# Kernel tuning notes

Hardware: AMD Instinct MI355X
Metric: run time of the kernel (lower is better)

## Reference

```python
import jax, jax.numpy as jnp
import numpy as np

N_HEADS = 8
D_EMBED = 64
B, S = 2, 2048
ROPE_BASE = 10000.0


def apply_rope(x):
    # x: [b, h, s, d]; interleaved-pair rotary embedding over the s axis
    d = x.shape[-1]
    s = x.shape[-2]
    inv_freq = 1.0 / (ROPE_BASE ** (jnp.arange(0, d, 2, dtype=jnp.float32) / d))  # [d/2]
    angles = jnp.arange(s, dtype=jnp.float32)[:, None] * inv_freq[None, :]  # [s, d/2]
    cos = jnp.cos(angles)[None, None, :, :]
    sin = jnp.sin(angles)[None, None, :, :]
    x1 = x[..., 0::2]
    x2 = x[..., 1::2]
    out = jnp.stack([x1 * cos - x2 * sin, x1 * sin + x2 * cos], axis=-1)
    return out.reshape(x.shape)


def setup_inputs() -> dict:
    key = jax.random.key(0)
    ks = jax.random.split(key, 7)
    scale = 1.0 / np.sqrt(D_EMBED)
    return {
        "q": jax.random.normal(ks[0], (B, S, D_EMBED), dtype=jnp.float32),
        "k": jax.random.normal(ks[1], (B, S, D_EMBED), dtype=jnp.float32),
        "v": jax.random.normal(ks[2], (B, S, D_EMBED), dtype=jnp.float32),
        "W_q": jax.random.normal(ks[3], (N_HEADS, D_EMBED, D_EMBED), dtype=jnp.float32) * scale,
        "W_k": jax.random.normal(ks[4], (N_HEADS, D_EMBED, D_EMBED), dtype=jnp.float32) * scale,
        "W_v": jax.random.normal(ks[5], (N_HEADS, D_EMBED, D_EMBED), dtype=jnp.float32) * scale,
        "W_o": jax.random.normal(ks[6], (N_HEADS * D_EMBED, D_EMBED), dtype=jnp.float32) * scale,
    }


def reference(q, k, v, W_q, W_k, W_v, W_o):
    Bn, Sn, E = q.shape
    H = W_q.shape[0]
    qh = jnp.einsum('bsz,hzd->bhsd', q, W_q)
    kh = jnp.einsum('bsz,hzd->bhsd', k, W_k)
    vh = jnp.einsum('bsz,hzd->bhsd', v, W_v)
    qh = apply_rope(qh)
    kh = apply_rope(kh)
    attn_scaling = 1.0 / E  # note: 1/d, not 1/sqrt(d), per original
    scores = jnp.einsum('bhqd,bhkd->bhqk', qh, kh)
    causal = jnp.triu(jnp.ones((Sn, Sn), dtype=bool), k=1)
    scores = jnp.where(causal[None, None], -jnp.inf, scores) * attn_scaling
    probs = jax.nn.softmax(scores, axis=-1)
    # post-softmax diagonal zeroing (breaks normalization; this is the ICL twist)
    diag_mask = 1.0 - jnp.eye(Sn, dtype=probs.dtype)
    probs = probs * diag_mask[None, None]
    # NOTE: einsum 'bhzs,bhzd->bhsd' in the original contracts over the QUERY axis
    # (probs transposed): out[k-pos] = sum_q P[q, k-pos] * v[q]
    out = jnp.einsum('bhqk,bhqd->bhkd', probs, vh)
    out = out.transpose(0, 2, 1, 3).reshape(Bn, Sn, H * E)
    return jnp.einsum('bsz,zd->bsd', out, W_o)
```

## Files before the change

### kernel.cpp

```cpp
#include <hip/hip_runtime.h>
#include <hip/hip_bf16.h>
#include <math.h>

#define NH 8
#define D 64
#define BB 2
#define SS 2048
#define NBH (BB*NH)
#define LOG2E 1.4426950408889634f
#define KPAR 8
#define QPAR 4

typedef short bf16x8 __attribute__((ext_vector_type(8)));
typedef float f32x4 __attribute__((ext_vector_type(4)));

#define MFMA16(a,b,c) __builtin_amdgcn_mfma_f32_16x16x32_bf16((a),(b),(c),0,0,0)

__device__ inline short f2bf(float f) {
    unsigned u = __float_as_uint(f);
    unsigned r = (u + 0x7fffu + ((u >> 16) & 1u)) >> 16;
    return (short)r;
}
__device__ inline float bf2f(short s) {
    return __uint_as_float(((unsigned)(unsigned short)s) << 16);
}
__device__ inline unsigned pack2bf(float a, float b) {
    __hip_bfloat162 hv = __float22bfloat162_rn(make_float2(a, b));
    unsigned u;
    __builtin_memcpy(&u, &hv, 4);
    return u;
}

__global__ __launch_bounds__(256) void wtrans_kernel(
    const float* __restrict__ Wq, const float* __restrict__ Wk,
    const float* __restrict__ Wv, const float* __restrict__ Wo,
    short* __restrict__ WqT, short* __restrict__ WkT, short* __restrict__ WvT,
    short* __restrict__ WoT) {
    int blk = blockIdx.x;
    int t = threadIdx.x;
    if (blk < 24) {
        int tensor = blk >> 3, h = blk & 7;
        const float* W = tensor == 0 ? Wq : (tensor == 1 ? Wk : Wv);
        short* WT = tensor == 0 ? WqT : (tensor == 1 ? WkT : WvT);
        __shared__ float wl[64][65];
        {
            int z = t >> 2, c0 = (t & 3) * 16;
            const float* src = W + (size_t)h * 4096 + (size_t)z * 64 + c0;
#pragma unroll
            for (int i = 0; i < 16; ++i) wl[z][c0 + i] = src[i];
        }
        __syncthreads();
        {
            int d = t >> 2, z0 = (t & 3) * 16;
            short* dst = WT + ((size_t)h * 64 + d) * 64 + z0;
#pragma unroll
            for (int i = 0; i < 16; ++i) dst[i] = f2bf(wl[z0 + i][d]);
        }
    } else {
        int idx = (blk - 24) * 256 + t;
        int d = idx >> 6;
        int zc = (idx & 63) * 32;
#pragma unroll
        for (int j = 0; j < 32; ++j) {
            int z = zc + j;
            WoT[(size_t)d * 2048 + z] = f2bf(Wo[(size_t)(z & 511) * 64 + d]);
        }
    }
}

__global__ __launch_bounds__(256) void proj_mfma_kernel(
    const float* __restrict__ xq, const float* __restrict__ xk,
    const float* __restrict__ xv,
    const short* __restrict__ WqT, const short* __restrict__ WkT,
    const short* __restrict__ WvT,
    short* __restrict__ qh, short* __restrict__ kh, short* __restrict__ vhT) {
    int blk = blockIdx.x;
    int tensor = blk / (NBH * 32);
    int rem = blk - tensor * (NBH * 32);
    int st = rem & 31, bh = rem >> 5;
    int h = bh & 7, b = bh >> 3;
    const float* x = tensor == 0 ? xq : (tensor == 1 ? xk : xv);
    const short* WT = tensor == 0 ? WqT : (tensor == 1 ? WkT : WvT);

    int t = threadIdx.x, w = t >> 6, lane = t & 63;
    int l15 = lane & 15, lg = lane >> 4;

    __shared__ short vt[64 * 64];

    int sA = st * 64 + w * 16 + l15;
    const float* xr = x + ((size_t)b * SS + sA) * D + lg * 8;
    bf16x8 a0, a1;
#pragma unroll
    for (int j = 0; j < 8; ++j) a0[j] = f2bf(xr[j]);
#pragma unroll
    for (int j = 0; j < 8; ++j) a1[j] = f2bf(xr[32 + j]);

    bf16x8 bfr[4][2];
#pragma unroll
    for (int ds_ = 0; ds_ < 4; ++ds_) {
        int d = ds_ * 16 + l15;
        const short* wp = WT + ((size_t)h * 64 + d) * 64 + lg * 8;
        bfr[ds_][0] = *(const bf16x8*)(wp);
        bfr[ds_][1] = *(const bf16x8*)(wp + 32);
    }

    f32x4 c[4];
#pragma unroll
    for (int ds_ = 0; ds_ < 4; ++ds_) {
        f32x4 z = {0.f, 0.f, 0.f, 0.f};
        z = MFMA16(a0, bfr[ds_][0], z);
        z = MFMA16(a1, bfr[ds_][1], z);
        c[ds_] = z;
    }

    int sbase = st * 64 + w * 16 + lg * 4;
    if (tensor < 2) {
        short* dst = tensor == 0 ? qh : kh;
        float scale = tensor == 0 ? (LOG2E / 64.0f) : 1.0f;
#pragma unroll
        for (int ds_ = 0; ds_ < 4; ++ds_) {
            int d = ds_ * 16 + l15;
            float invf = exp2f(-(float)(d & ~1) * (13.287712379549449f / 64.0f));
#pragma unroll
            for (int r = 0; r < 4; ++r) {
                float v = c[ds_][r];
                float pr = __shfl_xor(v, 1);
                float ang = (float)(sbase + r) * invf;
                float cs = __cosf(ang), sn = __sinf(ang);
                float o = (d & 1) ? (pr * sn + v * cs) : (v * cs - pr * sn);
                dst[((size_t)bh * SS + sbase + r) * D + d] = f2bf(o * scale);
            }
        }
    } else {
#pragma unroll
        for (int ds_ = 0; ds_ < 4; ++ds_) {
            int d = ds_ * 16 + l15;
#pragma unroll
            for (int r = 0; r < 4; ++r) {
                int sc = w * 16 + lg * 4 + r;
                vt[d * 64 + (sc ^ ((d & 7) << 3))] = f2bf(c[ds_][r]);
            }
        }
        __syncthreads();
#pragma unroll
        for (int pp = 0; pp < 2; ++pp) {
            int idx = pp * 256 + t;
            int d = idx >> 3, a = idx & 7;
            bf16x8 val = *(const bf16x8*)&vt[d * 64 + ((a ^ (d & 7)) << 3)];
            *(bf16x8*)&vhT[((size_t)bh * D + d) * SS + st * 64 + a * 8] = val;
        }
    }
}

__global__ __launch_bounds__(256, 4) void colstats_kernel(
    const short* __restrict__ qh, const short* __restrict__ kh,
    float* __restrict__ lpart) {
    int blk = blockIdx.x;
    int ph2 = blk & 1, qt = (blk >> 1) & 31, bh = blk >> 6;
    int t = threadIdx.x, w = t >> 6, lane = t & 63;
    int l15 = lane & 15, lg = lane >> 4;
    int pp = ph2 * 4 + w;

    bf16x8 qb[4][2];
#pragma unroll
    for (int qs = 0; qs < 4; ++qs) {
        const short* qp = qh + ((size_t)bh * SS + qt * 64 + qs * 16 + l15) * D + lg * 8;
        qb[qs][0] = *(const bf16x8*)qp;
        qb[qs][1] = *(const bf16x8*)(qp + 32);
    }

    const short* kbase = kh + (size_t)bh * SS * D;
    float lsum[4] = {0.f, 0.f, 0.f, 0.f};

    for (int kt = pp; kt <= qt; kt += KPAR) {
        bool diag = (kt == qt);
#pragma unroll
        for (int ks = 0; ks < 4; ++ks) {
            const short* kp = kbase + (size_t)(kt * 64 + ks * 16 + l15) * D + lg * 8;
            bf16x8 ka0 = *(const bf16x8*)kp;
            bf16x8 ka1 = *(const bf16x8*)(kp + 32);
            int kb = kt * 64 + ks * 16 + lg * 4;
#pragma unroll
            for (int qs = 0; qs < 4; ++qs) {
                f32x4 s = {0.f, 0.f, 0.f, 0.f};
                s = MFMA16(ka0, qb[qs][0], s);
                s = MFMA16(ka1, qb[qs][1], s);
                int qc = qt * 64 + qs * 16 + l15;
#pragma unroll
                for (int r = 0; r < 4; ++r) {
                    float e = (!diag || kb + r <= qc) ? exp2f(s[r]) : 0.f;
                    lsum[qs] += e;
                }
            }
        }
    }
#pragma unroll
    for (int qs = 0; qs < 4; ++qs) {
        lsum[qs] += __shfl_xor(lsum[qs], 16);
        lsum[qs] += __shfl_xor(lsum[qs], 32);
    }
    if (lane < 16) {
#pragma unroll
        for (int qs = 0; qs < 4; ++qs)
            lpart[((size_t)pp * NBH + bh) * SS + qt * 64 + qs * 16 + lane] = lsum[qs];
    }
}

__global__ __launch_bounds__(256) void merge_scale_kernel(
    const float* __restrict__ lpart, short* __restrict__ vhT) {
    int blk = blockIdx.x;
    int qc = blk & 15, bh = blk >> 4;
    int t = threadIdx.x;
    const size_t STR = (size_t)NBH * SS;
    __shared__ float il[128];
    if (t < 128) {
        size_t idx = (size_t)bh * SS + qc * 128 + t;
        float l = 0.f;
#pragma unroll
        for (int pp = 0; pp < KPAR; ++pp) l += lpart[pp * STR + idx];
        il[t] = 1.0f / l;
    }
    __syncthreads();
    int d = t >> 2, sub = t & 3;
    size_t base = ((size_t)bh * 64 + d) * SS + qc * 128 + sub * 32;
#pragma unroll
    for (int j = 0; j < 32; j += 8) {
        bf16x8 v = *(bf16x8*)&vhT[base + j];
#pragma unroll
        for (int jj = 0; jj < 8; ++jj)
            v[jj] = f2bf(bf2f(v[jj]) * il[sub * 32 + j + jj]);
        *(bf16x8*)&vhT[base + j] = v;
    }
}

__global__ __launch_bounds__(256, 4) void pv_kernel(
    const short* __restrict__ qh, const short* __restrict__ kh,
    const short* __restrict__ vhT,
    short* __restrict__ attc) {
    int blk = blockIdx.x;
    int ph = blk & 3, p = (blk >> 2) & 15, bh = blk >> 6;
    int h = bh & 7, b = bh >> 3;
    int t = threadIdx.x, w = t >> 6, lane = t & 63;
    int l15 = lane & 15, lg = lane >> 4;
    int kt = (w & 1) ? (31 - p) : p;
    int hf = w >> 1;
    int row0 = kt * 64 + hf * 32;

    __shared__ short pl[4][32 * 64];
    short* plw = pl[w];

    bf16x8 kb[2][2];
#pragma unroll
    for (int kg = 0; kg < 2; ++kg) {
        const short* kp = kh + ((size_t)bh * SS + row0 + kg * 16 + l15) * D + lg * 8;
        kb[kg][0] = *(const bf16x8*)kp;
        kb[kg][1] = *(const bf16x8*)(kp + 32);
    }

    f32x4 acc[2][4];
#pragma unroll
    for (int rg = 0; rg < 2; ++rg)
#pragma unroll
        for (int i = 0; i < 4; ++i) acc[rg][i] = (f32x4){0.f, 0.f, 0.f, 0.f};

    const short* qbase = qh + (size_t)bh * SS * D;
    const short* vbase = vhT + (size_t)bh * D * SS;

    int qt0 = kt + ((ph - kt) & (QPAR - 1));
    for (int qt = qt0; qt < 32; qt += QPAR) {
        bool diag = (qt == kt);
        bf16x8 qa[4][2];
#pragma unroll
        for (int qg = 0; qg < 4; ++qg) {
            const short* qp2 = qbase + (size_t)(qt * 64 + qg * 16 + l15) * D + lg * 8;
            qa[qg][0] = *(const bf16x8*)qp2;
            qa[qg][1] = *(const bf16x8*)(qp2 + 32);
        }
#pragma unroll
        for (int qg = 0; qg < 4; ++qg) {
#pragma unroll
            for (int kg = 0; kg < 2; ++kg) {
                f32x4 s = {0.f, 0.f, 0.f, 0.f};
                s = MFMA16(qa[qg][0], kb[kg][0], s);
                s = MFMA16(qa[qg][1], kb[kg][1], s);
                float p0 = exp2f(s[0]);
                float p1 = exp2f(s[1]);
                float p2 = exp2f(s[2]);
                float p3 = exp2f(s[3]);
                if (diag) {
                    int qoff = qg * 16 + 4 * lg;
                    int kk = hf * 32 + kg * 16 + l15;
                    if (qoff + 0 <= kk) p0 = 0.f;
                    if (qoff + 1 <= kk) p1 = 0.f;
                    if (qoff + 2 <= kk) p2 = 0.f;
                    if (qoff + 3 <= kk) p3 = 0.f;
                }
                unsigned u0 = pack2bf(p0, p1);
                unsigned u1 = pack2bf(p2, p3);
                int row = kg * 16 + l15;
                int col = (qg * 16 + 4 * lg) ^ ((row & 7) << 3);
                uint2 val;
                val.x = u0;
                val.y = u1;
                *(uint2*)&plw[row * 64 + col] = val;
            }
        }
#pragma unroll
        for (int qhh = 0; qhh < 2; ++qhh) {
            int chunk = (qhh << 2) | lg;
            int cc = (chunk ^ (l15 & 7)) << 3;
            bf16x8 pa0 = *(const bf16x8*)&plw[l15 * 64 + cc];
            bf16x8 pa1 = *(const bf16x8*)&plw[(16 + l15) * 64 + cc];
#pragma unroll
            for (int ds_ = 0; ds_ < 4; ++ds_) {
                const short* vp2 = vbase + (size_t)(ds_ * 16 + l15) * SS + qt * 64 + chunk * 8;
                bf16x8 vb = *(const bf16x8*)vp2;
                acc[0][ds_] = MFMA16(pa0, vb, acc[0][ds_]);
                acc[1][ds_] = MFMA16(pa1, vb, acc[1][ds_]);
            }
        }
    }
#pragma unroll
    for (int rg = 0; rg < 2; ++rg)
#pragma unroll
        for (int ds_ = 0; ds_ < 4; ++ds_) {
            int d = ds_ * 16 + l15;
#pragma unroll
            for (int r = 0; r < 4; ++r) {
                int k = row0 + rg * 16 + lg * 4 + r;
                attc[((size_t)b * SS + k) * 2048 + ph * 512 + h * 64 + d] =
                    f2bf(acc[rg][ds_][r]);
            }
        }
}

__global__ __launch_bounds__(256) void outproj_kernel(
    const short* __restrict__ attc, const short* __restrict__ WoT,
    float* __restrict__ out) {
    int blk = blockIdx.x;
    int t = threadIdx.x, w = t >> 6, lane = t & 63;
    int l15 = lane & 15, lg = lane >> 4;
    int srow = blk * 16 + l15;
    const short* arow = attc + (size_t)srow * 2048 + lg * 8;

    f32x4 acc[4];
#pragma unroll
    for (int i = 0; i < 4; ++i) acc[i] = (f32x4){0.f, 0.f, 0.f, 0.f};

#pragma unroll
    for (int i = 0; i < 16; ++i) {
        int kc = w * 16 + i;
        bf16x8 af = *(const bf16x8*)(arow + kc * 32);
#pragma unroll
        for (int ds_ = 0; ds_ < 4; ++ds_) {
            bf16x8 bf_ = *(const bf16x8*)&WoT[(size_t)(ds_ * 16 + l15) * 2048 + kc * 32 + lg * 8];
            acc[ds_] = MFMA16(af, bf_, acc[ds_]);
        }
    }
    __shared__ float red[4][16 * 64];
#pragma unroll
    for (int ds_ = 0; ds_ < 4; ++ds_)
#pragma unroll
        for (int r = 0; r < 4; ++r)
            red[w][(lg * 4 + r) * 64 + ds_ * 16 + l15] = acc[ds_][r];
    __syncthreads();
    {
        int idx4 = t * 4;
        int row = idx4 >> 6, col = idx4 & 63;
        float4 s0 = *(const float4*)&red[0][row * 64 + col];
        float4 s1 = *(const float4*)&red[1][row * 64 + col];
        float4 s2 = *(const float4*)&red[2][row * 64 + col];
        float4 s3 = *(const float4*)&red[3][row * 64 + col];
        float4 sum;
        sum.x = s0.x + s1.x + s2.x + s3.x;
        sum.y = s0.y + s1.y + s2.y + s3.y;
        sum.z = s0.z + s1.z + s2.z + s3.z;
        sum.w = s0.w + s1.w + s2.w + s3.w;
        *(float4*)&out[(size_t)(blk * 16 + row) * 64 + col] = sum;
    }
}

extern "C" void kernel_launch(void* const* d_in, const int* in_sizes, int n_in,
                              void* d_out, int out_size, void* d_ws, size_t ws_size,
                              hipStream_t stream) {
    const float* q  = (const float*)d_in[0];
    const float* k  = (const float*)d_in[1];
    const float* v  = (const float*)d_in[2];
    const float* Wq = (const float*)d_in[3];
    const float* Wk = (const float*)d_in[4];
    const float* Wv = (const float*)d_in[5];
    const float* Wo = (const float*)d_in[6];
    float* out = (float*)d_out;

    const size_t PROJ = (size_t)NBH * SS * D;

    short* qh  = (short*)d_ws;
    short* kh  = qh + PROJ;
    short* vhT = kh + PROJ;
    short* WqT = vhT + PROJ;
    short* WkT = WqT + 32768;
    short* WvT = WkT + 32768;
    short* WoT = WvT + 32768;
    float* lpart = (float*)(WoT + 131072);
    short* attc  = (short*)(lpart + (size_t)KPAR * NBH * SS);

    wtrans_kernel<<<40, 256, 0, stream>>>(Wq, Wk, Wv, Wo, WqT, WkT, WvT, WoT);

    proj_mfma_kernel<<<3 * NBH * 32, 256, 0, stream>>>(q, k, v, WqT, WkT, WvT,
                                                       qh, kh, vhT);

    colstats_kernel<<<NBH * 64, 256, 0, stream>>>(qh, kh, lpart);

    merge_scale_kernel<<<NBH * 16, 256, 0, stream>>>(lpart, vhT);

    pv_kernel<<<NBH * 64, 256, 0, stream>>>(qh, kh, vhT, attc);

    outproj_kernel<<<256, 256, 0, stream>>>(attc, WoT, out);
}
```

Measured before the change: 103.5 us.

## Split colstats and PV work across more blocks with in-block wave reduction

KPAR is doubled so colstats launches twice as many blocks, each covering a finer stride of key tiles and writing more partial sums. pv_kernel now gives each block a single key tile rather than pairing kt with 31-kt. Two waves per row-half take interleaved query-tile classes (stride 8), and their accumulators are summed through LDS before the bf16 store. This raises the block count and shortens per-block serial loops. In exchange it drops the triangular load-balancing pairing, adds an LDS reduction with two barriers, and makes merge_scale read more partials.

```diff
diff --git a/kernel.cpp b/kernel.cpp
--- a/kernel.cpp
+++ b/kernel.cpp
@@ -8,8 +8,8 @@
 #define SS 2048
 #define NBH (BB*NH)
 #define LOG2E 1.4426950408889634f
-#define KPAR 8
-#define QPAR 4
+#define KPAR 16
+#define QCLS 8
 
 typedef short bf16x8 __attribute__((ext_vector_type(8)));
 typedef float f32x4 __attribute__((ext_vector_type(4)));
@@ -156,10 +156,10 @@
     const short* __restrict__ qh, const short* __restrict__ kh,
     float* __restrict__ lpart) {
     int blk = blockIdx.x;
-    int ph2 = blk & 1, qt = (blk >> 1) & 31, bh = blk >> 6;
+    int ph4 = blk & 3, qt = (blk >> 2) & 31, bh = blk >> 7;
     int t = threadIdx.x, w = t >> 6, lane = t & 63;
     int l15 = lane & 15, lg = lane >> 4;
-    int pp = ph2 * 4 + w;
+    int pp = ph4 * 4 + w;
 
     bf16x8 qb[4][2];
 #pragma unroll
@@ -238,12 +238,12 @@
     const short* __restrict__ vhT,
     short* __restrict__ attc) {
     int blk = blockIdx.x;
-    int ph = blk & 3, p = (blk >> 2) & 15, bh = blk >> 6;
+    int ph = blk & 3, kt = (blk >> 2) & 31, bh = blk >> 7;
     int h = bh & 7, b = bh >> 3;
     int t = threadIdx.x, w = t >> 6, lane = t & 63;
     int l15 = lane & 15, lg = lane >> 4;
-    int kt = (w & 1) ? (31 - p) : p;
-    int hf = w >> 1;
+    int sp = w & 1, hf = w >> 1;
+    int qcls = ph * 2 + sp;
     int row0 = kt * 64 + hf * 32;
 
     __shared__ short pl[4][32 * 64];
@@ -266,8 +266,8 @@
     const short* qbase = qh + (size_t)bh * SS * D;
     const short* vbase = vhT + (size_t)bh * D * SS;
 
-    int qt0 = kt + ((ph - kt) & (QPAR - 1));
-    for (int qt = qt0; qt < 32; qt += QPAR) {
+    int qt0 = kt + ((qcls - kt) & (QCLS - 1));
+    for (int qt = qt0; qt < 32; qt += QCLS) {
         bool diag = (qt == kt);
         bf16x8 qa[4][2];
 #pragma unroll
@@ -320,18 +320,36 @@
             }
         }
     }
-#pragma unroll
-    for (int rg = 0; rg < 2; ++rg)
-#pragma unroll
-        for (int ds_ = 0; ds_ < 4; ++ds_) {
-            int d = ds_ * 16 + l15;
-#pragma unroll
-            for (int r = 0; r < 4; ++r) {
-                int k = row0 + rg * 16 + lg * 4 + r;
-                attc[((size_t)b * SS + k) * 2048 + ph * 512 + h * 64 + d] =
-                    f2bf(acc[rg][ds_][r]);
-            }
-        }
+
+    __syncthreads();
+    float* plf = (float*)pl;
+    if (sp == 1) {
+#pragma unroll
+        for (int rg = 0; rg < 2; ++rg)
+#pragma unroll
+            for (int ds_ = 0; ds_ < 4; ++ds_) {
+                int d = ds_ * 16 + l15;
+#pragma unroll
+                for (int r = 0; r < 4; ++r)
+                    plf[hf * 2048 + (rg * 16 + lg * 4 + r) * 64 + d] = acc[rg][ds_][r];
+            }
+    }
+    __syncthreads();
+    if (sp == 0) {
+#pragma unroll
+        for (int rg = 0; rg < 2; ++rg)
+#pragma unroll
+            for (int ds_ = 0; ds_ < 4; ++ds_) {
+                int d = ds_ * 16 + l15;
+#pragma unroll
+                for (int r = 0; r < 4; ++r) {
+                    int lrow = rg * 16 + lg * 4 + r;
+                    float sum = acc[rg][ds_][r] + plf[hf * 2048 + lrow * 64 + d];
+                    int k = row0 + lrow;
+                    attc[((size_t)b * SS + k) * 2048 + ph * 512 + h * 64 + d] = f2bf(sum);
+                }
+            }
+    }
 }
 
 __global__ __launch_bounds__(256) void outproj_kernel(
@@ -409,11 +427,11 @@
     proj_mfma_kernel<<<3 * NBH * 32, 256, 0, stream>>>(q, k, v, WqT, WkT, WvT,
                                                        qh, kh, vhT);
 
-    colstats_kernel<<<NBH * 64, 256, 0, stream>>>(qh, kh, lpart);
+    colstats_kernel<<<NBH * 128, 256, 0, stream>>>(qh, kh, lpart);
 
     merge_scale_kernel<<<NBH * 16, 256, 0, stream>>>(lpart, vhT);
 
-    pv_kernel<<<NBH * 64, 256, 0, stream>>>(qh, kh, vhT, attc);
+    pv_kernel<<<NBH * 128, 256, 0, stream>>>(qh, kh, vhT, attc);
 
     outproj_kernel<<<256, 256, 0, stream>>>(attc, WoT, out);
 }
```

Result: slower. 117.6 us (+13.6%).

## Double-buffer K/Q loads and split pv query range across waves with LDS reduction

Applied to the files above, without the earlier changes.

The row-sum kernel now double-buffers K tile loads so the next tile's global reads are issued before the current tile's MFMAs and exp2. The pv kernel is restructured so each block processes both the kt=p and kt=31-p tiles in sequence. Pairs of waves split the query tiles into 8 classes and their partial accumulators are reduced through shared memory before the bf16 store, with half of each Q tile prefetched ahead. The aim is to hide memory latency and balance causal work, at the cost of extra syncthreads, LDS traffic and register pressure.

```diff
diff --git a/kernel.cpp b/kernel.cpp
--- a/kernel.cpp
+++ b/kernel.cpp
@@ -9,7 +9,7 @@
 #define NBH (BB*NH)
 #define LOG2E 1.4426950408889634f
 #define KPAR 8
-#define QPAR 4
+#define QCLS 8
 
 typedef short bf16x8 __attribute__((ext_vector_type(8)));
 typedef float f32x4 __attribute__((ext_vector_type(4)));
@@ -172,19 +172,24 @@
     const short* kbase = kh + (size_t)bh * SS * D;
     float lsum[4] = {0.f, 0.f, 0.f, 0.f};
 
-    for (int kt = pp; kt <= qt; kt += KPAR) {
-        bool diag = (kt == qt);
+    auto load_k = [&](bf16x8 (&ka)[4][2], int kt) {
 #pragma unroll
         for (int ks = 0; ks < 4; ++ks) {
             const short* kp = kbase + (size_t)(kt * 64 + ks * 16 + l15) * D + lg * 8;
-            bf16x8 ka0 = *(const bf16x8*)kp;
-            bf16x8 ka1 = *(const bf16x8*)(kp + 32);
+            ka[ks][0] = *(const bf16x8*)kp;
+            ka[ks][1] = *(const bf16x8*)(kp + 32);
+        }
+    };
+    auto compute = [&](bf16x8 (&ka)[4][2], int kt) {
+        bool diag = (kt == qt);
+#pragma unroll
+        for (int ks = 0; ks < 4; ++ks) {
             int kb = kt * 64 + ks * 16 + lg * 4;
 #pragma unroll
             for (int qs = 0; qs < 4; ++qs) {
                 f32x4 s = {0.f, 0.f, 0.f, 0.f};
-                s = MFMA16(ka0, qb[qs][0], s);
-                s = MFMA16(ka1, qb[qs][1], s);
+                s = MFMA16(ka[ks][0], qb[qs][0], s);
+                s = MFMA16(ka[ks][1], qb[qs][1], s);
                 int qc = qt * 64 + qs * 16 + l15;
 #pragma unroll
                 for (int r = 0; r < 4; ++r) {
@@ -192,6 +197,24 @@
                     lsum[qs] += e;
                 }
             }
+        }
+    };
+
+    bf16x8 kaA[4][2], kaB[4][2];
+    int kt = pp;
+    if (kt <= qt) {
+        load_k(kaA, kt);
+        while (true) {
+            int ktn = kt + KPAR;
+            if (ktn <= qt) load_k(kaB, ktn);
+            compute(kaA, kt);
+            kt = ktn;
+            if (kt > qt) break;
+            ktn = kt + KPAR;
+            if (ktn <= qt) load_k(kaA, ktn);
+            compute(kaB, kt);
+            kt = ktn;
+            if (kt > qt) break;
         }
     }
 #pragma unroll
@@ -242,96 +265,152 @@
     int h = bh & 7, b = bh >> 3;
     int t = threadIdx.x, w = t >> 6, lane = t & 63;
     int l15 = lane & 15, lg = lane >> 4;
-    int kt = (w & 1) ? (31 - p) : p;
-    int hf = w >> 1;
-    int row0 = kt * 64 + hf * 32;
+    int qsub = w & 1, hf = w >> 1;
+    int qcls = ph * 2 + qsub;
 
     __shared__ short pl[4][32 * 64];
     short* plw = pl[w];
-
-    bf16x8 kb[2][2];
-#pragma unroll
-    for (int kg = 0; kg < 2; ++kg) {
-        const short* kp = kh + ((size_t)bh * SS + row0 + kg * 16 + l15) * D + lg * 8;
-        kb[kg][0] = *(const bf16x8*)kp;
-        kb[kg][1] = *(const bf16x8*)(kp + 32);
-    }
-
-    f32x4 acc[2][4];
-#pragma unroll
-    for (int rg = 0; rg < 2; ++rg)
-#pragma unroll
-        for (int i = 0; i < 4; ++i) acc[rg][i] = (f32x4){0.f, 0.f, 0.f, 0.f};
+    float* red = (float*)pl;
 
     const short* qbase = qh + (size_t)bh * SS * D;
     const short* vbase = vhT + (size_t)bh * D * SS;
 
-    int qt0 = kt + ((ph - kt) & (QPAR - 1));
-    for (int qt = qt0; qt < 32; qt += QPAR) {
-        bool diag = (qt == kt);
-        bf16x8 qa[4][2];
-#pragma unroll
-        for (int qg = 0; qg < 4; ++qg) {
-            const short* qp2 = qbase + (size_t)(qt * 64 + qg * 16 + l15) * D + lg * 8;
-            qa[qg][0] = *(const bf16x8*)qp2;
-            qa[qg][1] = *(const bf16x8*)(qp2 + 32);
-        }
-#pragma unroll
-        for (int qg = 0; qg < 4; ++qg) {
-#pragma unroll
-            for (int kg = 0; kg < 2; ++kg) {
-                f32x4 s = {0.f, 0.f, 0.f, 0.f};
-                s = MFMA16(qa[qg][0], kb[kg][0], s);
-                s = MFMA16(qa[qg][1], kb[kg][1], s);
-                float p0 = exp2f(s[0]);
-                float p1 = exp2f(s[1]);
-                float p2 = exp2f(s[2]);
-                float p3 = exp2f(s[3]);
-                if (diag) {
-                    int qoff = qg * 16 + 4 * lg;
-                    int kk = hf * 32 + kg * 16 + l15;
-                    if (qoff + 0 <= kk) p0 = 0.f;
-                    if (qoff + 1 <= kk) p1 = 0.f;
-                    if (qoff + 2 <= kk) p2 = 0.f;
-                    if (qoff + 3 <= kk) p3 = 0.f;
+    for (int it = 0; it < 2; ++it) {
+        if (it) __syncthreads();
+        int kt = it ? (31 - p) : p;
+        int row0 = kt * 64 + hf * 32;
+
+        bf16x8 kb[2][2];
+#pragma unroll
+        for (int kg = 0; kg < 2; ++kg) {
+            const short* kp = kh + ((size_t)bh * SS + row0 + kg * 16 + l15) * D + lg * 8;
+            kb[kg][0] = *(const bf16x8*)kp;
+            kb[kg][1] = *(const bf16x8*)(kp + 32);
+        }
+
+        f32x4 acc[2][4];
+#pragma unroll
+        for (int rg = 0; rg < 2; ++rg)
+#pragma unroll
+            for (int i = 0; i < 4; ++i) acc[rg][i] = (f32x4){0.f, 0.f, 0.f, 0.f};
+
+        auto load_pre = [&](bf16x8 (&qp)[2][2], int qt) {
+#pragma unroll
+            for (int qg = 0; qg < 2; ++qg) {
+                const short* qp2 = qbase + (size_t)(qt * 64 + qg * 16 + l15) * D + lg * 8;
+                qp[qg][0] = *(const bf16x8*)qp2;
+                qp[qg][1] = *(const bf16x8*)(qp2 + 32);
+            }
+        };
+        auto qk_phase = [&](bf16x8 (&qp)[2][2], int qt) {
+            bool diag = (qt == kt);
+            bf16x8 q2[2][2];
+#pragma unroll
+            for (int j = 0; j < 2; ++j) {
+                const short* qp2 = qbase + (size_t)(qt * 64 + (2 + j) * 16 + l15) * D + lg * 8;
+                q2[j][0] = *(const bf16x8*)qp2;
+                q2[j][1] = *(const bf16x8*)(qp2 + 32);
+            }
+#pragma unroll
+            for (int qg = 0; qg < 4; ++qg) {
+                bf16x8* qa = (qg < 2) ? &qp[qg][0] : &q2[qg - 2][0];
+#pragma unroll
+                for (int kg = 0; kg < 2; ++kg) {
+                    f32x4 s = {0.f, 0.f, 0.f, 0.f};
+                    s = MFMA16(qa[0], kb[kg][0], s);
+                    s = MFMA16(qa[1], kb[kg][1], s);
+                    float p0 = exp2f(s[0]);
+                    float p1 = exp2f(s[1]);
+                    float p2 = exp2f(s[2]);
+                    float p3 = exp2f(s[3]);
+                    if (diag) {
+                        int qoff = qg * 16 + 4 * lg;
+                        int kk = hf * 32 + kg * 16 + l15;
+                        if (qoff + 0 <= kk) p0 = 0.f;
+                        if (qoff + 1 <= kk) p1 = 0.f;
+                        if (qoff + 2 <= kk) p2 = 0.f;
+                        if (qoff + 3 <= kk) p3 = 0.f;
+                    }
+                    unsigned u0 = pack2bf(p0, p1);
+                    unsigned u1 = pack2bf(p2, p3);
+                    int row = kg * 16 + l15;
+                    int col = (qg * 16 + 4 * lg) ^ ((row & 7) << 3);
+                    uint2 val;
+                    val.x = u0;
+                    val.y = u1;
+                    *(uint2*)&plw[row * 64 + col] = val;
                 }
-                unsigned u0 = pack2bf(p0, p1);
-                unsigned u1 = pack2bf(p2, p3);
-                int row = kg * 16 + l15;
-                int col = (qg * 16 + 4 * lg) ^ ((row & 7) << 3);
-                uint2 val;
-                val.x = u0;
-                val.y = u1;
-                *(uint2*)&plw[row * 64 + col] = val;
-            }
-        }
-#pragma unroll
-        for (int qhh = 0; qhh < 2; ++qhh) {
-            int chunk = (qhh << 2) | lg;
-            int cc = (chunk ^ (l15 & 7)) << 3;
-            bf16x8 pa0 = *(const bf16x8*)&plw[l15 * 64 + cc];
-            bf16x8 pa1 = *(const bf16x8*)&plw[(16 + l15) * 64 + cc];
-#pragma unroll
-            for (int ds_ = 0; ds_ < 4; ++ds_) {
-                const short* vp2 = vbase + (size_t)(ds_ * 16 + l15) * SS + qt * 64 + chunk * 8;
-                bf16x8 vb = *(const bf16x8*)vp2;
-                acc[0][ds_] = MFMA16(pa0, vb, acc[0][ds_]);
-                acc[1][ds_] = MFMA16(pa1, vb, acc[1][ds_]);
-            }
-        }
-    }
-#pragma unroll
-    for (int rg = 0; rg < 2; ++rg)
-#pragma unroll
-        for (int ds_ = 0; ds_ < 4; ++ds_) {
-            int d = ds_ * 16 + l15;
-#pragma unroll
-            for (int r = 0; r < 4; ++r) {
-                int k = row0 + rg * 16 + lg * 4 + r;
-                attc[((size_t)b * SS + k) * 2048 + ph * 512 + h * 64 + d] =
-                    f2bf(acc[rg][ds_][r]);
-            }
-        }
+            }
+        };
+        auto pv_phase = [&](int qt) {
+#pragma unroll
+            for (int qhh = 0; qhh < 2; ++qhh) {
+                int chunk = (qhh << 2) | lg;
+                int cc = (chunk ^ (l15 & 7)) << 3;
+                bf16x8 pa0 = *(const bf16x8*)&plw[l15 * 64 + cc];
+                bf16x8 pa1 = *(const bf16x8*)&plw[(16 + l15) * 64 + cc];
+#pragma unroll
+                for (int ds_ = 0; ds_ < 4; ++ds_) {
+                    const short* vp2 = vbase + (size_t)(ds_ * 16 + l15) * SS + qt * 64 + chunk * 8;
+                    bf16x8 vb = *(const bf16x8*)vp2;
+                    acc[0][ds_] = MFMA16(pa0, vb, acc[0][ds_]);
+                    acc[1][ds_] = MFMA16(pa1, vb, acc[1][ds_]);
+                }
+            }
+        };
+
+        int qt0 = kt + ((qcls - kt) & (QCLS - 1));
+        bf16x8 qpA[2][2], qpB[2][2];
+        int qt = qt0;
+        if (qt < 32) {
+            load_pre(qpA, qt);
+            while (true) {
+                qk_phase(qpA, qt);
+                int qtn = qt + QCLS;
+                if (qtn < 32) load_pre(qpB, qtn);
+                pv_phase(qt);
+                qt = qtn;
+                if (qt >= 32) break;
+                qk_phase(qpB, qt);
+                qtn = qt + QCLS;
+                if (qtn < 32) load_pre(qpA, qtn);
+                pv_phase(qt);
+                qt = qtn;
+                if (qt >= 32) break;
+            }
+        }
+
+        __syncthreads();
+        if (qsub == 1) {
+#pragma unroll
+            for (int rg = 0; rg < 2; ++rg)
+#pragma unroll
+                for (int ds_ = 0; ds_ < 4; ++ds_) {
+                    int dd = ds_ * 16 + l15;
+#pragma unroll
+                    for (int r = 0; r < 4; ++r) {
+                        int lrow = rg * 16 + lg * 4 + r;
+                        red[hf * 2048 + lrow * 64 + (dd ^ (lg << 3))] = acc[rg][ds_][r];
+                    }
+                }
+        }
+        __syncthreads();
+        if (qsub == 0) {
+#pragma unroll
+            for (int rg = 0; rg < 2; ++rg)
+#pragma unroll
+                for (int ds_ = 0; ds_ < 4; ++ds_) {
+                    int dd = ds_ * 16 + l15;
+#pragma unroll
+                    for (int r = 0; r < 4; ++r) {
+                        int lrow = rg * 16 + lg * 4 + r;
+                        float sum = acc[rg][ds_][r] + red[hf * 2048 + lrow * 64 + (dd ^ (lg << 3))];
+                        int k = row0 + lrow;
+                        attc[((size_t)b * SS + k) * 2048 + ph * 512 + h * 64 + dd] = f2bf(sum);
+                    }
+                }
+        }
+    }
 }
 
 __global__ __launch_bounds__(256) void outproj_kernel(
```

Result: slower. 126.1 us (+21.8%).
